# Optimization experiments

Measured on AMD Instinct MI355X. Metric: run time of the kernel, lower is better.

## Reference

```python
import jax, jax.numpy as jnp
import numpy as np
import math

B, L, D, H = 4, 1024, 512, 8
TAU = 0.1
LN_EPS = 1e-5


def _attn(xq, xk, xv, wq, bq, wk, bk, wv, bv, wo, bo, energy=None, threshold=None):
    Bq, Lq, Dm = xq.shape
    Dh = Dm // H
    Q = (xq @ wq.T + bq).reshape(Bq, Lq, H, Dh)
    K = (xk @ wk.T + bk).reshape(Bq, -1, H, Dh)
    V = (xv @ wv.T + bv).reshape(Bq, -1, H, Dh)
    sc = jnp.einsum('bqhd,bkhd->bhqk', Q, K) / jnp.sqrt(jnp.float32(Dh))
    if energy is not None:
        # mask keys whose mean |energy| over channels is below threshold
        mask = jnp.abs(energy).mean(-1)[:, None, None, :] > threshold  # (B,1,1,Lk)
        sc = jnp.where(mask, sc, -jnp.inf)
    w = jnp.nan_to_num(jax.nn.softmax(sc, axis=-1))  # nan->0 for fully-masked rows
    o = jnp.einsum('bhqk,bkhd->bqhd', w, V).reshape(Bq, Lq, Dm)
    return o @ wo.T + bo


def _ln(x, w, b):
    m = x.mean(-1, keepdims=True)
    v = x.var(-1, keepdims=True)
    return (x - m) / jnp.sqrt(v + LN_EPS) * w + b


def _mlp(x, w1, b1, w2, b2):
    h = jax.nn.gelu(x @ w1.T + b1, approximate=False)  # torch nn.GELU default = exact
    return h @ w2.T + b2


def setup_inputs():
    key = jax.random.key(0)
    ks = list(jax.random.split(key, 64))

    def nxt():
        return ks.pop(0)

    def w(shape, scale=0.02):
        return jax.random.normal(nxt(), shape, dtype=jnp.float32) * scale

    inp = {
        'LL': jax.random.normal(nxt(), (B, D, L), dtype=jnp.float32),
        'LH': jax.random.normal(nxt(), (B, D, L), dtype=jnp.float32),
        'raw_tau': jnp.float32(math.log(TAU / (1.0 - TAU))),
    }
    for p in ('llA', 'lhA', 'crA'):
        for nm in ('q', 'k', 'v', 'o'):
            inp[f'{p}_w{nm}'] = w((D, D))
            inp[f'{p}_b{nm}'] = jnp.zeros((D,), jnp.float32)
    for p in ('mlp_ll', 'mlp_lh'):
        inp[f'{p}_w1'] = w((4 * D, D))
        inp[f'{p}_b1'] = jnp.zeros((4 * D,), jnp.float32)
        inp[f'{p}_w2'] = w((D, 4 * D))
        inp[f'{p}_b2'] = jnp.zeros((D,), jnp.float32)
    inp['n1_w'] = jnp.ones((D,), jnp.float32)
    inp['n1_b'] = jnp.zeros((D,), jnp.float32)
    inp['n2_w'] = jnp.ones((D,), jnp.float32)
    inp['n2_b'] = jnp.zeros((D,), jnp.float32)
    return inp


def reference(LL, LH, raw_tau,
              llA_wq, llA_bq, llA_wk, llA_bk, llA_wv, llA_bv, llA_wo, llA_bo,
              lhA_wq, lhA_bq, lhA_wk, lhA_bk, lhA_wv, lhA_bv, lhA_wo, lhA_bo,
              crA_wq, crA_bq, crA_wk, crA_bk, crA_wv, crA_bv, crA_wo, crA_bo,
              mlp_ll_w1, mlp_ll_b1, mlp_ll_w2, mlp_ll_b2,
              mlp_lh_w1, mlp_lh_b1, mlp_lh_w2, mlp_lh_b2,
              n1_w, n1_b, n2_w, n2_b):
    tau = jax.nn.sigmoid(raw_tau)
    ll_s = jnp.transpose(LL, (0, 2, 1))  # (B,L,D)
    lh_s = jnp.transpose(LH, (0, 2, 1))
    ll_o = _attn(ll_s, ll_s, ll_s, llA_wq, llA_bq, llA_wk, llA_bk, llA_wv, llA_bv, llA_wo, llA_bo)
    lh_o = _attn(lh_s, lh_s, lh_s, lhA_wq, lhA_bq, lhA_wk, lhA_bk, lhA_wv, lhA_bv, lhA_wo, lhA_bo,
                 energy=lh_s, threshold=tau)
    cr_o = _attn(ll_o, lh_o, lh_o, crA_wq, crA_bq, crA_wk, crA_bk, crA_wv, crA_bv, crA_wo, crA_bo)
    ll_f = _ln(ll_s + ll_o + cr_o, n1_w, n1_b)
    ll_f = _mlp(ll_f, mlp_ll_w1, mlp_ll_b1, mlp_ll_w2, mlp_ll_b2) + ll_f
    lh_f = _ln(lh_s + lh_o, n2_w, n2_b)
    lh_f = _mlp(lh_f, mlp_lh_w1, mlp_lh_b1, mlp_lh_w2, mlp_lh_b2) + lh_f
    return (jnp.transpose(ll_f, (0, 2, 1)), jnp.transpose(lh_f, (0, 2, 1)))
```

## Files before the change

kernel.cpp:

```cpp
#include <hip/hip_runtime.h>
#include <hip/hip_bf16.h>
#include <stdint.h>

typedef unsigned short u16;
typedef __bf16 bf16_t;
typedef bf16_t bf16x8 __attribute__((ext_vector_type(8)));
typedef float f32x4 __attribute__((ext_vector_type(4)));

#define DEV static __device__ __forceinline__

DEV u16 f2b(float f) {
    __hip_bfloat16 h = __float2bfloat16(f);
    return __builtin_bit_cast(u16, h);
}

DEV bf16x8 ld_frag(const u16* p) {
    uint4 u = *reinterpret_cast<const uint4*>(p);
    return __builtin_bit_cast(bf16x8, u);
}

DEV float gelu(float v) {
    float y = 0.79788456080286536f * (v + 0.044715f * v * v * v);
    float e = __expf(-2.f * fabsf(y));
    float th = (1.f - e) / (1.f + e);
    th = copysignf(th, y);
    return 0.5f * v * (1.f + th);
}

DEV void gl_lds16(const u16* g, u16* l) {
    __builtin_amdgcn_global_load_lds(
        (const __attribute__((address_space(1))) void*)(uintptr_t)g,
        (__attribute__((address_space(3))) void*)(unsigned int)(uintptr_t)l,
        16, 0, 0);
}

struct ConvEnt { const float* s; u16* d; int n; };
struct CpyEnt { const float* s; float* d; };
struct PreArgs {
    const float* LL; const float* LH;
    float* llf; u16* llb; float* lhf; u16* lhb;
    ConvEnt ce[16];
    CpyEnt pe[8];
};

__global__ __launch_bounds__(256) void k_pre(PreArgs a) {
    __shared__ float tb[32][33];
    const int bid = blockIdx.x, t = threadIdx.x;
    if (bid < 4096) {
        const int z = bid >> 9, gy = (bid >> 5) & 15, gx = bid & 31;
        const int b = z & 3;
        const float* in = (z < 4) ? a.LL : a.LH;
        float* of = (z < 4) ? a.llf : a.lhf;
        u16* ob = (z < 4) ? a.llb : a.lhb;
        const int l0 = gx * 32, d0 = gy * 32;
        const int tx = t & 31, ty = t >> 5;
#pragma unroll
        for (int j = 0; j < 4; ++j) {
            int d = d0 + ty + j * 8;
            tb[ty + j * 8][tx] = in[((size_t)b * 512 + d) * 1024 + l0 + tx];
        }
        __syncthreads();
#pragma unroll
        for (int j = 0; j < 4; ++j) {
            int l = l0 + ty + j * 8;
            float v = tb[tx][ty + j * 8];
            size_t o = ((size_t)b * 1024 + l) * 512 + d0 + tx;
            of[o] = v;
            ob[o] = f2b(v);
        }
    } else if (bid < 8192) {
        const int cb = bid - 4096;
        const ConvEnt en = a.ce[cb >> 8];
        for (int i = ((cb & 255) * 256 + t) * 4; i < en.n; i += 256 * 256 * 4) {
            const float4 f = *reinterpret_cast<const float4*>(en.s + i);
            unsigned r0 = (unsigned)f2b(f.x) | ((unsigned)f2b(f.y) << 16);
            unsigned r1 = (unsigned)f2b(f.z) | ((unsigned)f2b(f.w) << 16);
            uint2 rr; rr.x = r0; rr.y = r1;
            *reinterpret_cast<uint2*>(en.d + i) = rr;
        }
    } else {
        const int cb = bid - 8192;
        const CpyEnt en = a.pe[cb >> 1];
        const int i = (cb & 1) * 256 + t;
        en.d[i] = en.s[i];
    }
}

__global__ __launch_bounds__(256) void k_tout(const float* __restrict__ y0, const float* __restrict__ y1,
                                              float* __restrict__ out) {
    __shared__ float tb[32][33];
    int z = blockIdx.z, b = z & 3;
    const float* in = (z < 4) ? y0 : y1;
    float* o = out + ((z < 4) ? 0 : (size_t)4096 * 512);
    int l0 = blockIdx.x * 32, d0 = blockIdx.y * 32;
    int tx = threadIdx.x, ty = threadIdx.y;
#pragma unroll
    for (int j = 0; j < 4; ++j) {
        int l = l0 + ty + j * 8;
        tb[ty + j * 8][tx] = in[((size_t)b * 1024 + l) * 512 + d0 + tx];
    }
    __syncthreads();
#pragma unroll
    for (int j = 0; j < 4; ++j) {
        int d = d0 + ty + j * 8;
        o[((size_t)b * 512 + d) * 1024 + l0 + tx] = tb[tx][ty + j * 8];
    }
}

__global__ __launch_bounds__(256) void k_mask(const float* __restrict__ lh_s,
                                              const float* __restrict__ raw_tau,
                                              float* __restrict__ kbias) {
    int row = blockIdx.x * 4 + (threadIdx.x >> 6);
    int lane = threadIdx.x & 63;
    const float* p = lh_s + (size_t)row * 512 + lane * 8;
    float s = 0.f;
#pragma unroll
    for (int j = 0; j < 8; ++j) s += fabsf(p[j]);
#pragma unroll
    for (int m = 32; m >= 1; m >>= 1) s += __shfl_xor(s, m, 64);
    float tau = 1.f / (1.f + expf(-raw_tau[0]));
    if (lane == 0) kbias[row] = (s * (1.f / 512.f) > tau) ? 0.f : -3.0e38f;
}

__global__ __launch_bounds__(256) void k_ln(const float* __restrict__ a, const float* __restrict__ b,
                                            const float* __restrict__ c, const float* __restrict__ w,
                                            const float* __restrict__ bi,
                                            float* __restrict__ of, u16* __restrict__ ob) {
    int row = blockIdx.x * 4 + (threadIdx.x >> 6);
    int lane = threadIdx.x & 63;
    size_t base = (size_t)row * 512 + lane * 8;
    float x[8];
#pragma unroll
    for (int j = 0; j < 8; ++j) {
        float v = a[base + j] + b[base + j];
        if (c) v += c[base + j];
        x[j] = v;
    }
    float s = 0.f, s2 = 0.f;
#pragma unroll
    for (int j = 0; j < 8; ++j) { s += x[j]; s2 += x[j] * x[j]; }
#pragma unroll
    for (int m = 32; m >= 1; m >>= 1) { s += __shfl_xor(s, m, 64); s2 += __shfl_xor(s2, m, 64); }
    float mean = s * (1.f / 512.f);
    float var = s2 * (1.f / 512.f) - mean * mean;
    float rs = rsqrtf(var + 1e-5f);
#pragma unroll
    for (int j = 0; j < 8; ++j) {
        float y = (x[j] - mean) * rs * w[lane * 8 + j] + bi[lane * 8 + j];
        of[base + j] = y;
        ob[base + j] = f2b(y);
    }
}

struct GP {
    const u16* A; const u16* W; const float* bias; const float* res;
    float* Cf; u16* Cb; u16* Qp; u16* Kp; u16* Vt;
    int N, K, kB, vB, nwg;
};

template <int BM, int BN, int GELU_ACT, int PACK>
__global__ __launch_bounds__(256) void k_gemm(GP p0, GP p1, int M) {
    constexpr int BK = 64;
    __shared__ alignas(16) u16 Al[2][BM * BK];
    __shared__ alignas(16) u16 Wl[2][BN * BK];
    GP g = (blockIdx.y == 0) ? p0 : p1;
    const int orig = blockIdx.x;
    if (orig >= g.nwg) return;
    int bid;
    {
        const int xcd = orig & 7, lin = orig >> 3;
        const int q = g.nwg >> 3, r = g.nwg & 7;
        bid = (xcd < r ? xcd * (q + 1) : r * (q + 1) + (xcd - r) * q) + lin;
    }
    const int K = g.K, N = g.N;
    const int nny = N / BN;
    const int m0 = (bid / nny) * BM, n0 = (bid % nny) * BN;

    const int t = threadIdx.x, w = t >> 6, l = t & 63;
    constexpr int FM = BM / 32, FN = BN / 32;
    const int wr = w >> 1, wc = w & 1;
    const int lq = l & 15, lg = l >> 4;
    f32x4 acc[FM][FN] = {};

    const int srow = l >> 3, schunk = l & 7;
    auto stage = [&](int kcol, int buf) {
#pragma unroll
        for (int i = 0; i < BM / 32; ++i) {
            const int row = i * 32 + w * 8 + srow;
            gl_lds16(g.A + (size_t)(m0 + row) * K + kcol + ((schunk ^ (row & 7)) * 8),
                     &Al[buf][(i * 32 + w * 8) * BK]);
        }
#pragma unroll
        for (int i = 0; i < BN / 32; ++i) {
            const int row = i * 32 + w * 8 + srow;
            gl_lds16(g.W + (size_t)(n0 + row) * K + kcol + ((schunk ^ (row & 7)) * 8),
                     &Wl[buf][(i * 32 + w * 8) * BK]);
        }
    };

    stage(0, 0);
    const int KT = K / BK;
    for (int kt = 0; kt < KT; ++kt) {
        const int cur = kt & 1;
        __syncthreads();
        if (kt + 1 < KT) stage((kt + 1) * BK, cur ^ 1);
#pragma unroll
        for (int s = 0; s < 2; ++s) {
            bf16x8 af[FM], bw[FN];
#pragma unroll
            for (int i = 0; i < FM; ++i) {
                const int row = wr * (BM / 2) + i * 16 + lq;
                af[i] = ld_frag(&Al[cur][row * BK + (((s * 4 + lg) ^ (row & 7)) * 8)]);
            }
#pragma unroll
            for (int j = 0; j < FN; ++j) {
                const int row = wc * (BN / 2) + j * 16 + lq;
                bw[j] = ld_frag(&Wl[cur][row * BK + (((s * 4 + lg) ^ (row & 7)) * 8)]);
            }
#pragma unroll
            for (int i = 0; i < FM; ++i)
#pragma unroll
                for (int j = 0; j < FN; ++j)
                    acc[i][j] = __builtin_amdgcn_mfma_f32_16x16x32_bf16(af[i], bw[j], acc[i][j], 0, 0, 0);
        }
    }

    if (PACK && n0 >= g.vB) {
        u16* T = (u16*)Al;
        constexpr int CH = BM / 8, CMASK = CH - 1, SH = (CH == 16) ? 4 : 3;
        __syncthreads();
#pragma unroll
        for (int i = 0; i < FM; ++i) {
#pragma unroll
            for (int j = 0; j < FN; ++j) {
                const int ni = wc * (BN / 2) + j * 16 + lq;
                const float bn = g.bias[n0 + ni];
#pragma unroll
                for (int r2 = 0; r2 < 4; ++r2) {
                    const int mi = wr * (BM / 2) + i * 16 + lg * 4 + r2;
                    T[ni * BM + (((mi >> 3) ^ (ni & CMASK)) * 8) + (mi & 7)] = f2b(acc[i][j][r2] + bn);
                }
            }
        }
        __syncthreads();
        const int bb = m0 >> 10, mloc = m0 & 1023;
        const int mc = t & CMASK, nib = t >> SH;
        constexpr int RPP = 256 / CH;
#pragma unroll
        for (int p2 = 0; p2 < BN / RPP; ++p2) {
            const int ni = nib + p2 * RPP;
            uint4 u = *reinterpret_cast<const uint4*>(&T[ni * BM + ((mc ^ (ni & CMASK)) * 8)]);
            const int d = n0 - g.vB + ni;
            *reinterpret_cast<uint4*>(
                &g.Vt[((size_t)(bb * 8 + (d >> 6)) * 64 + (d & 63)) * 1024 + mloc + mc * 8]) = u;
        }
        return;
    }

#pragma unroll
    for (int i = 0; i < FM; ++i) {
#pragma unroll
        for (int j = 0; j < FN; ++j) {
            const int n = n0 + wc * (BN / 2) + j * 16 + lq;
            const float bn = g.bias[n];
#pragma unroll
            for (int r2 = 0; r2 < 4; ++r2) {
                const int m = m0 + wr * (BM / 2) + i * 16 + lg * 4 + r2;
                float v = acc[i][j][r2] + bn;
                if (GELU_ACT) v = gelu(v);
                if (PACK) {
                    const int bb = m >> 10, ll_ = m & 1023;
                    if (n >= g.kB) {
                        const int d = n - g.kB;
                        g.Kp[((size_t)(bb * 8 + (d >> 6)) * 1024 + ll_) * 64 + (d & 63)] = f2b(v);
                    } else {
                        g.Qp[((size_t)(bb * 8 + (n >> 6)) * 1024 + ll_) * 64 + (n & 63)] = f2b(v * 0.125f);
                    }
                } else {
                    size_t o = (size_t)m * N + n;
                    if (g.res) v += g.res[o];
                    if (g.Cf) g.Cf[o] = v;
                    if (g.Cb) g.Cb[o] = f2b(v);
                }
            }
        }
    }
}

__global__ __launch_bounds__(256) void k_attn(const u16* __restrict__ Qp, const u16* __restrict__ Kp,
                                              const u16* __restrict__ Vtp, u16* __restrict__ O,
                                              const float* __restrict__ kbias, int nwg) {
    constexpr int L = 1024;
    __shared__ alignas(16) u16 Kl[2][64 * 64];
    __shared__ alignas(16) u16 Vl[2][64 * 64];
    __shared__ alignas(16) u16 Pl[128 * 64];
    const int t = threadIdx.x, w = t >> 6, l = t & 63;
    const int bid = ((int)blockIdx.x & 7) * (nwg >> 3) + ((int)blockIdx.x >> 3);
    const int bh = bid >> 3, q0 = (bid & 7) * 128;
    const int bz = bh >> 3, h = bh & 7;
    const int lq = l & 15, lg = l >> 4;
    const float* kb = (kbias != nullptr && bz >= 4) ? (kbias + (size_t)(bz - 4) * L) : nullptr;

    bf16x8 qa[2][2];
#pragma unroll
    for (int i = 0; i < 2; ++i) {
        const u16* qp = Qp + ((size_t)bh * L + q0 + w * 32 + i * 16 + lq) * 64 + lg * 8;
        qa[i][0] = ld_frag(qp);
        qa[i][1] = ld_frag(qp + 32);
    }

    const int r0 = w * 16 + (l >> 3), r1 = r0 + 8, c = l & 7;
    const u16* Ksrc0 = Kp + (size_t)bh * L * 64 + (size_t)r0 * 64 + ((c ^ (r0 & 7)) * 8);
    const u16* Ksrc1 = Kp + (size_t)bh * L * 64 + (size_t)r1 * 64 + ((c ^ (r1 & 7)) * 8);
    const u16* Vsrc0 = Vtp + (size_t)bh * 64 * L + (size_t)r0 * L + ((c ^ (r0 & 7)) * 8);
    const u16* Vsrc1 = Vtp + (size_t)bh * 64 * L + (size_t)r1 * L + ((c ^ (r1 & 7)) * 8);

    auto stage = [&](int k0, int buf) {
        gl_lds16(Ksrc0 + (size_t)k0 * 64, &Kl[buf][(w * 16) * 64]);
        gl_lds16(Ksrc1 + (size_t)k0 * 64, &Kl[buf][(w * 16 + 8) * 64]);
        gl_lds16(Vsrc0 + k0, &Vl[buf][(w * 16) * 64]);
        gl_lds16(Vsrc1 + k0, &Vl[buf][(w * 16 + 8) * 64]);
    };

    int addrA[4][2];
#pragma unroll
    for (int f = 0; f < 4; ++f) {
        int row = f * 16 + lq;
#pragma unroll
        for (int s = 0; s < 2; ++s) addrA[f][s] = row * 64 + (((s * 4 + lg) ^ (row & 7)) * 8);
    }
    int pwr[2][4], paddr[2][2];
#pragma unroll
    for (int i = 0; i < 2; ++i) {
        const int q = w * 32 + i * 16 + lq;
#pragma unroll
        for (int f = 0; f < 4; ++f) {
            const int chunk = f * 2 + (lg >> 1);
            pwr[i][f] = q * 64 + ((chunk ^ (lq & 7)) * 8) + (lg & 1) * 4;
        }
#pragma unroll
        for (int s = 0; s < 2; ++s) paddr[i][s] = q * 64 + (((s * 4 + lg) ^ (lq & 7)) * 8);
    }

    f32x4 oacc[2][4] = {};
    float lsum[2] = {0.f, 0.f};

    stage(0, 0);
    for (int kt = 0; kt < 16; ++kt) {
        const int cur = kt & 1;
        __syncthreads();
        if (kt + 1 < 16) stage((kt + 1) * 64, cur ^ 1);

        f32x4 sc[2][4];
#pragma unroll
        for (int f = 0; f < 4; ++f) {
            bf16x8 k0 = ld_frag(&Kl[cur][addrA[f][0]]);
            bf16x8 k1 = ld_frag(&Kl[cur][addrA[f][1]]);
#pragma unroll
            for (int i = 0; i < 2; ++i) {
                f32x4 a = {};
                a = __builtin_amdgcn_mfma_f32_16x16x32_bf16(k0, qa[i][0], a, 0, 0, 0);
                a = __builtin_amdgcn_mfma_f32_16x16x32_bf16(k1, qa[i][1], a, 0, 0, 0);
                sc[i][f] = a;
            }
        }
#pragma unroll
        for (int f = 0; f < 4; ++f) {
            float4 bv4;
            if (kb) bv4 = *reinterpret_cast<const float4*>(kb + kt * 64 + f * 16 + lg * 4);
            else { bv4.x = 0.f; bv4.y = 0.f; bv4.z = 0.f; bv4.w = 0.f; }
#pragma unroll
            for (int i = 0; i < 2; ++i) {
                float p0 = __expf(sc[i][f][0] + bv4.x);
                float p1 = __expf(sc[i][f][1] + bv4.y);
                float p2 = __expf(sc[i][f][2] + bv4.z);
                float p3 = __expf(sc[i][f][3] + bv4.w);
                lsum[i] += (p0 + p1) + (p2 + p3);
                uint2 pk;
                pk.x = (unsigned)f2b(p0) | ((unsigned)f2b(p1) << 16);
                pk.y = (unsigned)f2b(p2) | ((unsigned)f2b(p3) << 16);
                *reinterpret_cast<uint2*>(&Pl[pwr[i][f]]) = pk;
            }
        }
        bf16x8 pa[2][2];
#pragma unroll
        for (int i = 0; i < 2; ++i) {
            pa[i][0] = ld_frag(&Pl[paddr[i][0]]);
            pa[i][1] = ld_frag(&Pl[paddr[i][1]]);
        }
#pragma unroll
        for (int db = 0; db < 4; ++db) {
            bf16x8 v0 = ld_frag(&Vl[cur][addrA[db][0]]);
            bf16x8 v1 = ld_frag(&Vl[cur][addrA[db][1]]);
#pragma unroll
            for (int i = 0; i < 2; ++i) {
                oacc[i][db] = __builtin_amdgcn_mfma_f32_16x16x32_bf16(pa[i][0], v0, oacc[i][db], 0, 0, 0);
                oacc[i][db] = __builtin_amdgcn_mfma_f32_16x16x32_bf16(pa[i][1], v1, oacc[i][db], 0, 0, 0);
            }
        }
    }
#pragma unroll
    for (int i = 0; i < 2; ++i) {
        float v = lsum[i];
        v += __shfl_xor(v, 16, 64);
        v += __shfl_xor(v, 32, 64);
        lsum[i] = v;
    }
#pragma unroll
    for (int i = 0; i < 2; ++i) {
        float inv[4];
#pragma unroll
        for (int r = 0; r < 4; ++r) {
            float den = __shfl(lsum[i], lg * 4 + r, 64);
            inv[r] = (den > 0.f) ? 1.f / den : 0.f;
        }
#pragma unroll
        for (int db = 0; db < 4; ++db) {
#pragma unroll
            for (int r = 0; r < 4; ++r) {
                O[((size_t)bz * L + q0 + w * 32 + i * 16 + lg * 4 + r) * 512 + h * 64 + db * 16 + lq] =
                    f2b(oacc[i][db][r] * inv[r]);
            }
        }
    }
}

extern "C" void kernel_launch(void* const* d_in, const int* in_sizes, int n_in,
                              void* d_out, int out_size, void* d_ws, size_t ws_size,
                              hipStream_t stream) {
    const int M = 4096;
    const float* LL = (const float*)d_in[0];
    const float* LH = (const float*)d_in[1];
    const float* raw_tau = (const float*)d_in[2];
    auto F = [&](int i) { return (const float*)d_in[i]; };
    const int BIG = 1 << 28;

    char* p = (char*)d_ws;
    auto alloc = [&](size_t bytes) { void* r = (void*)p; p += (bytes + 255) & ~(size_t)255; return r; };
    const size_t MDf = (size_t)M * 512 * 4, MDb = (size_t)M * 512 * 2;
    float* ll_s_f = (float*)alloc(MDf);
    float* lh_s_f = (float*)alloc(MDf);
    u16* ll_s_b = (u16*)alloc(MDb);
    u16* lh_s_b = (u16*)alloc(MDb);
    u16* Qp = (u16*)alloc(2 * MDb);
    u16* Kp = (u16*)alloc(2 * MDb);
    u16* Vt = (u16*)alloc(2 * MDb);
    u16* Cxb = (u16*)alloc(2 * MDb);
    float* ll_o_f = (float*)alloc(MDf);
    u16* ll_o_b = (u16*)alloc(MDb);
    float* lh_o_f = (float*)alloc(MDf);
    u16* lh_o_b = (u16*)alloc(MDb);
    float* cr_o_f = (float*)alloc(MDf);
    float* ln_f_ll = (float*)alloc(MDf);
    float* ln_f_lh = (float*)alloc(MDf);
    u16* ln_b = (u16*)alloc(MDb);
    u16* hb = (u16*)alloc((size_t)M * 2048 * 2);
    float* yf_ll = (float*)alloc(MDf);
    float* yf_lh = (float*)alloc(MDf);
    float* kbias = (float*)alloc(4096 * 4);
    float* bqkv_ll = (float*)alloc(1536 * 4);
    float* bqkv_lh = (float*)alloc(1536 * 4);
    float* bkv_cr = (float*)alloc(1024 * 4);
    const size_t WDD = (size_t)262144;
    u16* wqkv_ll = (u16*)alloc(3 * WDD * 2);
    u16* wqkv_lh = (u16*)alloc(3 * WDD * 2);
    u16* wkv_cr = (u16*)alloc(2 * WDD * 2);
    u16* wq_cr = (u16*)alloc(WDD * 2);
    u16* wo_ll = (u16*)alloc(WDD * 2);
    u16* wo_lh = (u16*)alloc(WDD * 2);
    u16* wo_cr = (u16*)alloc(WDD * 2);
    u16* wm[4];
    for (int i = 0; i < 4; ++i) wm[i] = (u16*)alloc((size_t)1048576 * 2);

    const size_t SET = (size_t)4 * 8 * 1024 * 64;

    PreArgs pa;
    pa.LL = LL; pa.LH = LH;
    pa.llf = ll_s_f; pa.llb = ll_s_b; pa.lhf = lh_s_f; pa.lhb = lh_s_b;
    pa.ce[0] = {F(3), wqkv_ll, (int)WDD};
    pa.ce[1] = {F(5), wqkv_ll + WDD, (int)WDD};
    pa.ce[2] = {F(7), wqkv_ll + 2 * WDD, (int)WDD};
    pa.ce[3] = {F(11), wqkv_lh, (int)WDD};
    pa.ce[4] = {F(13), wqkv_lh + WDD, (int)WDD};
    pa.ce[5] = {F(15), wqkv_lh + 2 * WDD, (int)WDD};
    pa.ce[6] = {F(19), wq_cr, (int)WDD};
    pa.ce[7] = {F(21), wkv_cr, (int)WDD};
    pa.ce[8] = {F(23), wkv_cr + WDD, (int)WDD};
    pa.ce[9] = {F(9), wo_ll, (int)WDD};
    pa.ce[10] = {F(17), wo_lh, (int)WDD};
    pa.ce[11] = {F(25), wo_cr, (int)WDD};
    pa.ce[12] = {F(27), wm[0], 1048576};
    pa.ce[13] = {F(29), wm[1], 1048576};
    pa.ce[14] = {F(31), wm[2], 1048576};
    pa.ce[15] = {F(33), wm[3], 1048576};
    pa.pe[0] = {F(4), bqkv_ll};
    pa.pe[1] = {F(6), bqkv_ll + 512};
    pa.pe[2] = {F(8), bqkv_ll + 1024};
    pa.pe[3] = {F(12), bqkv_lh};
    pa.pe[4] = {F(14), bqkv_lh + 512};
    pa.pe[5] = {F(16), bqkv_lh + 1024};
    pa.pe[6] = {F(22), bkv_cr};
    pa.pe[7] = {F(24), bkv_cr + 512};
    k_pre<<<dim3(8208), 256, 0, stream>>>(pa);
    k_mask<<<dim3(1024), 256, 0, stream>>>(lh_s_f, raw_tau, kbias);

    auto gp = [&](const u16* A, const u16* W, const float* bias, int N, int K, int nwg) {
        GP g = {};
        g.A = A; g.W = W; g.bias = bias; g.N = N; g.K = K; g.nwg = nwg;
        g.kB = BIG; g.vB = BIG;
        return g;
    };

    {
        GP a = gp(ll_s_b, wqkv_ll, bqkv_ll, 1536, 512, 384);
        a.kB = 512; a.vB = 1024; a.Qp = Qp; a.Kp = Kp; a.Vt = Vt;
        GP b = gp(lh_s_b, wqkv_lh, bqkv_lh, 1536, 512, 384);
        b.kB = 512; b.vB = 1024; b.Qp = Qp + SET; b.Kp = Kp + SET; b.Vt = Vt + SET;
        k_gemm<128, 128, 0, 1><<<dim3(384, 2), 256, 0, stream>>>(a, b, M);
    }
    k_attn<<<dim3(512), 256, 0, stream>>>(Qp, Kp, Vt, Cxb, kbias, 512);
    {
        GP a = gp(Cxb, wo_ll, F(10), 512, 512, 512);
        a.Cf = ll_o_f; a.Cb = ll_o_b;
        GP b = gp(Cxb + SET, wo_lh, F(18), 512, 512, 512);
        b.Cf = lh_o_f; b.Cb = lh_o_b;
        k_gemm<64, 64, 0, 0><<<dim3(512, 2), 256, 0, stream>>>(a, b, M);
    }
    k_ln<<<dim3(1024), 256, 0, stream>>>(lh_s_f, lh_o_f, nullptr, F(37), F(38), ln_f_lh, ln_b);
    {
        GP a = gp(ln_b, wm[2], F(32), 2048, 512, 512);
        a.Cb = hb;
        k_gemm<128, 128, 1, 0><<<dim3(512, 1), 256, 0, stream>>>(a, a, M);
    }
    {
        GP a = gp(ll_o_b, wq_cr, F(20), 512, 512, 512);
        a.Qp = Qp;
        GP b = gp(lh_o_b, wkv_cr, bkv_cr, 1024, 512, 1024);
        b.kB = 0; b.vB = 512; b.Kp = Kp; b.Vt = Vt;
        k_gemm<64, 64, 0, 1><<<dim3(1024, 2), 256, 0, stream>>>(a, b, M);
    }
    k_attn<<<dim3(256), 256, 0, stream>>>(Qp, Kp, Vt, Cxb, nullptr, 256);
    {
        GP a = gp(Cxb, wo_cr, F(26), 512, 512, 512);
        a.Cf = cr_o_f;
        GP b = gp(hb, wm[3], F(34), 512, 2048, 512);
        b.Cf = yf_lh; b.res = ln_f_lh;
        k_gemm<64, 64, 0, 0><<<dim3(512, 2), 256, 0, stream>>>(a, b, M);
    }
    k_ln<<<dim3(1024), 256, 0, stream>>>(ll_s_f, ll_o_f, cr_o_f, F(35), F(36), ln_f_ll, ln_b);
    {
        GP a = gp(ln_b, wm[0], F(28), 2048, 512, 512);
        a.Cb = hb;
        k_gemm<128, 128, 1, 0><<<dim3(512, 1), 256, 0, stream>>>(a, a, M);
    }
    {
        GP a = gp(hb, wm[1], F(30), 512, 2048, 512);
        a.Cf = yf_ll; a.res = ln_f_ll;
        k_gemm<64, 64, 0, 0><<<dim3(512, 1), 256, 0, stream>>>(a, a, M);
    }
    k_tout<<<dim3(32, 16, 8), dim3(32, 8), 0, stream>>>(yf_ll, yf_lh, (float*)d_out);
}
```

Measured before the change: 261.7 us.

## Fuse mask into pre kernel, merge GEMM launches, write transposed output from GEMM

```diff
diff --git a/kernel.cpp b/kernel.cpp
--- a/kernel.cpp
+++ b/kernel.cpp
@@ -39,6 +39,7 @@
 struct PreArgs {
     const float* LL; const float* LH;
     float* llf; u16* llb; float* lhf; u16* lhb;
+    const float* raw_tau; float* kbias;
     ConvEnt ce[16];
     CpyEnt pe[8];
 };
@@ -78,48 +79,27 @@
             uint2 rr; rr.x = r0; rr.y = r1;
             *reinterpret_cast<uint2*>(en.d + i) = rr;
         }
-    } else {
+    } else if (bid < 8208) {
         const int cb = bid - 8192;
         const CpyEnt en = a.pe[cb >> 1];
         const int i = (cb & 1) * 256 + t;
         en.d[i] = en.s[i];
-    }
-}
-
-__global__ __launch_bounds__(256) void k_tout(const float* __restrict__ y0, const float* __restrict__ y1,
-                                              float* __restrict__ out) {
-    __shared__ float tb[32][33];
-    int z = blockIdx.z, b = z & 3;
-    const float* in = (z < 4) ? y0 : y1;
-    float* o = out + ((z < 4) ? 0 : (size_t)4096 * 512);
-    int l0 = blockIdx.x * 32, d0 = blockIdx.y * 32;
-    int tx = threadIdx.x, ty = threadIdx.y;
-#pragma unroll
-    for (int j = 0; j < 4; ++j) {
-        int l = l0 + ty + j * 8;
-        tb[ty + j * 8][tx] = in[((size_t)b * 1024 + l) * 512 + d0 + tx];
-    }
-    __syncthreads();
-#pragma unroll
-    for (int j = 0; j < 4; ++j) {
-        int d = d0 + ty + j * 8;
-        o[((size_t)b * 512 + d) * 1024 + l0 + tx] = tb[tx][ty + j * 8];
-    }
-}
-
-__global__ __launch_bounds__(256) void k_mask(const float* __restrict__ lh_s,
-                                              const float* __restrict__ raw_tau,
-                                              float* __restrict__ kbias) {
-    int row = blockIdx.x * 4 + (threadIdx.x >> 6);
-    int lane = threadIdx.x & 63;
-    const float* p = lh_s + (size_t)row * 512 + lane * 8;
-    float s = 0.f;
-#pragma unroll
-    for (int j = 0; j < 8; ++j) s += fabsf(p[j]);
-#pragma unroll
-    for (int m = 32; m >= 1; m >>= 1) s += __shfl_xor(s, m, 64);
-    float tau = 1.f / (1.f + expf(-raw_tau[0]));
-    if (lane == 0) kbias[row] = (s * (1.f / 512.f) > tau) ? 0.f : -3.0e38f;
+    } else {
+        const int cb = bid - 8208;
+        const int b = cb >> 4, k = (cb & 15) * 64 + (t & 63);
+        const int dg = t >> 6;
+        float s = 0.f;
+        for (int d = dg * 128; d < dg * 128 + 128; ++d)
+            s += fabsf(a.LH[((size_t)b * 512 + d) * 1024 + k]);
+        float* ps = &tb[0][0];
+        ps[dg * 64 + (t & 63)] = s;
+        __syncthreads();
+        if (t < 64) {
+            float tot = ps[t] + ps[64 + t] + ps[128 + t] + ps[192 + t];
+            float tau = 1.f / (1.f + expf(-a.raw_tau[0]));
+            a.kbias[b * 1024 + (cb & 15) * 64 + t] = (tot * (1.f / 512.f) > tau) ? 0.f : -3.0e38f;
+        }
+    }
 }
 
 __global__ __launch_bounds__(256) void k_ln(const float* __restrict__ a, const float* __restrict__ b,
@@ -154,16 +134,16 @@
 
 struct GP {
     const u16* A; const u16* W; const float* bias; const float* res;
-    float* Cf; u16* Cb; u16* Qp; u16* Kp; u16* Vt;
-    int N, K, kB, vB, nwg;
+    float* Cf; u16* Cb; float* Ct; u16* Qp; u16* Kp; u16* Vt;
+    int N, K, kB, vB, nwg, gelu, pack;
 };
 
-template <int BM, int BN, int GELU_ACT, int PACK>
-__global__ __launch_bounds__(256) void k_gemm(GP p0, GP p1, int M) {
+template <int BM, int BN>
+__global__ __launch_bounds__(256) void k_gemm(GP p0, GP p1, GP p2, int M) {
     constexpr int BK = 64;
     __shared__ alignas(16) u16 Al[2][BM * BK];
     __shared__ alignas(16) u16 Wl[2][BN * BK];
-    GP g = (blockIdx.y == 0) ? p0 : p1;
+    GP g = (blockIdx.y == 0) ? p0 : (blockIdx.y == 1) ? p1 : p2;
     const int orig = blockIdx.x;
     if (orig >= g.nwg) return;
     int bid;
@@ -225,7 +205,7 @@
         }
     }
 
-    if (PACK && n0 >= g.vB) {
+    if (g.pack && n0 >= g.vB) {
         u16* T = (u16*)Al;
         constexpr int CH = BM / 8, CMASK = CH - 1, SH = (CH == 16) ? 4 : 3;
         __syncthreads();
@@ -263,20 +243,39 @@
         for (int j = 0; j < FN; ++j) {
             const int n = n0 + wc * (BN / 2) + j * 16 + lq;
             const float bn = g.bias[n];
+            const int mb = m0 + wr * (BM / 2) + i * 16 + lg * 4;
+            float vv[4];
 #pragma unroll
             for (int r2 = 0; r2 < 4; ++r2) {
-                const int m = m0 + wr * (BM / 2) + i * 16 + lg * 4 + r2;
                 float v = acc[i][j][r2] + bn;
-                if (GELU_ACT) v = gelu(v);
-                if (PACK) {
+                if (g.gelu) v = gelu(v);
+                vv[r2] = v;
+            }
+            if (g.pack) {
+#pragma unroll
+                for (int r2 = 0; r2 < 4; ++r2) {
+                    const int m = mb + r2;
                     const int bb = m >> 10, ll_ = m & 1023;
                     if (n >= g.kB) {
                         const int d = n - g.kB;
-                        g.Kp[((size_t)(bb * 8 + (d >> 6)) * 1024 + ll_) * 64 + (d & 63)] = f2b(v);
+                        g.Kp[((size_t)(bb * 8 + (d >> 6)) * 1024 + ll_) * 64 + (d & 63)] = f2b(vv[r2]);
                     } else {
-                        g.Qp[((size_t)(bb * 8 + (n >> 6)) * 1024 + ll_) * 64 + (n & 63)] = f2b(v * 0.125f);
+                        g.Qp[((size_t)(bb * 8 + (n >> 6)) * 1024 + ll_) * 64 + (n & 63)] = f2b(vv[r2] * 0.125f);
                     }
-                } else {
+                }
+            } else if (g.Ct) {
+                float4 o4;
+                o4.x = vv[0] + (g.res ? g.res[(size_t)(mb + 0) * N + n] : 0.f);
+                o4.y = vv[1] + (g.res ? g.res[(size_t)(mb + 1) * N + n] : 0.f);
+                o4.z = vv[2] + (g.res ? g.res[(size_t)(mb + 2) * N + n] : 0.f);
+                o4.w = vv[3] + (g.res ? g.res[(size_t)(mb + 3) * N + n] : 0.f);
+                *reinterpret_cast<float4*>(
+                    &g.Ct[((size_t)(mb >> 10) * 512 + n) * 1024 + (mb & 1023)]) = o4;
+            } else {
+#pragma unroll
+                for (int r2 = 0; r2 < 4; ++r2) {
+                    const int m = mb + r2;
+                    float v = vv[r2];
                     size_t o = (size_t)m * N + n;
                     if (g.res) v += g.res[o];
                     if (g.Cf) g.Cf[o] = v;
@@ -455,8 +454,6 @@
     float* ln_f_lh = (float*)alloc(MDf);
     u16* ln_b = (u16*)alloc(MDb);
     u16* hb = (u16*)alloc((size_t)M * 2048 * 2);
-    float* yf_ll = (float*)alloc(MDf);
-    float* yf_lh = (float*)alloc(MDf);
     float* kbias = (float*)alloc(4096 * 4);
     float* bqkv_ll = (float*)alloc(1536 * 4);
     float* bqkv_lh = (float*)alloc(1536 * 4);
@@ -477,6 +474,7 @@
     PreArgs pa;
     pa.LL = LL; pa.LH = LH;
     pa.llf = ll_s_f; pa.llb = ll_s_b; pa.lhf = lh_s_f; pa.lhb = lh_s_b;
+    pa.raw_tau = raw_tau; pa.kbias = kbias;
     pa.ce[0] = {F(3), wqkv_ll, (int)WDD};
     pa.ce[1] = {F(5), wqkv_ll + WDD, (int)WDD};
     pa.ce[2] = {F(7), wqkv_ll + 2 * WDD, (int)WDD};
@@ -501,8 +499,7 @@
     pa.pe[5] = {F(16), bqkv_lh + 1024};
     pa.pe[6] = {F(22), bkv_cr};
     pa.pe[7] = {F(24), bkv_cr + 512};
-    k_pre<<<dim3(8208), 256, 0, stream>>>(pa);
-    k_mask<<<dim3(1024), 256, 0, stream>>>(lh_s_f, raw_tau, kbias);
+    k_pre<<<dim3(8272), 256, 0, stream>>>(pa);
 
     auto gp = [&](const u16* A, const u16* W, const float* bias, int N, int K, int nwg) {
         GP g = {};
@@ -513,10 +510,10 @@
 
     {
         GP a = gp(ll_s_b, wqkv_ll, bqkv_ll, 1536, 512, 384);
-        a.kB = 512; a.vB = 1024; a.Qp = Qp; a.Kp = Kp; a.Vt = Vt;
+        a.pack = 1; a.kB = 512; a.vB = 1024; a.Qp = Qp; a.Kp = Kp; a.Vt = Vt;
         GP b = gp(lh_s_b, wqkv_lh, bqkv_lh, 1536, 512, 384);
-        b.kB = 512; b.vB = 1024; b.Qp = Qp + SET; b.Kp = Kp + SET; b.Vt = Vt + SET;
-        k_gemm<128, 128, 0, 1><<<dim3(384, 2), 256, 0, stream>>>(a, b, M);
+        b.pack = 1; b.kB = 512; b.vB = 1024; b.Qp = Qp + SET; b.Kp = Kp + SET; b.Vt = Vt + SET;
+        k_gemm<128, 128><<<dim3(384, 2), 256, 0, stream>>>(a, b, b, M);
     }
     k_attn<<<dim3(512), 256, 0, stream>>>(Qp, Kp, Vt, Cxb, kbias, 512);
     {
@@ -524,39 +521,35 @@
         a.Cf = ll_o_f; a.Cb = ll_o_b;
         GP b = gp(Cxb + SET, wo_lh, F(18), 512, 512, 512);
         b.Cf = lh_o_f; b.Cb = lh_o_b;
-        k_gemm<64, 64, 0, 0><<<dim3(512, 2), 256, 0, stream>>>(a, b, M);
+        k_gemm<64, 64><<<dim3(512, 2), 256, 0, stream>>>(a, b, b, M);
     }
     k_ln<<<dim3(1024), 256, 0, stream>>>(lh_s_f, lh_o_f, nullptr, F(37), F(38), ln_f_lh, ln_b);
     {
-        GP a = gp(ln_b, wm[2], F(32), 2048, 512, 512);
-        a.Cb = hb;
-        k_gemm<128, 128, 1, 0><<<dim3(512, 1), 256, 0, stream>>>(a, a, M);
-    }
-    {
-        GP a = gp(ll_o_b, wq_cr, F(20), 512, 512, 512);
-        a.Qp = Qp;
-        GP b = gp(lh_o_b, wkv_cr, bkv_cr, 1024, 512, 1024);
-        b.kB = 0; b.vB = 512; b.Kp = Kp; b.Vt = Vt;
-        k_gemm<64, 64, 0, 1><<<dim3(1024, 2), 256, 0, stream>>>(a, b, M);
+        GP a = gp(ln_b, wm[2], F(32), 2048, 512, 1024);
+        a.gelu = 1; a.Cb = hb;
+        GP b = gp(ll_o_b, wq_cr, F(20), 512, 512, 256);
+        b.pack = 1; b.Qp = Qp;
+        GP cd = gp(lh_o_b, wkv_cr, bkv_cr, 1024, 512, 512);
+        cd.pack = 1; cd.kB = 0; cd.vB = 512; cd.Kp = Kp; cd.Vt = Vt;
+        k_gemm<128, 64><<<dim3(1024, 3), 256, 0, stream>>>(a, b, cd, M);
     }
     k_attn<<<dim3(256), 256, 0, stream>>>(Qp, Kp, Vt, Cxb, nullptr, 256);
     {
         GP a = gp(Cxb, wo_cr, F(26), 512, 512, 512);
         a.Cf = cr_o_f;
         GP b = gp(hb, wm[3], F(34), 512, 2048, 512);
-        b.Cf = yf_lh; b.res = ln_f_lh;
-        k_gemm<64, 64, 0, 0><<<dim3(512, 2), 256, 0, stream>>>(a, b, M);
+        b.res = ln_f_lh; b.Ct = (float*)d_out + (size_t)4096 * 512;
+        k_gemm<64, 64><<<dim3(512, 2), 256, 0, stream>>>(a, b, b, M);
     }
     k_ln<<<dim3(1024), 256, 0, stream>>>(ll_s_f, ll_o_f, cr_o_f, F(35), F(36), ln_f_ll, ln_b);
     {
         GP a = gp(ln_b, wm[0], F(28), 2048, 512, 512);
-        a.Cb = hb;
-        k_gemm<128, 128, 1, 0><<<dim3(512, 1), 256, 0, stream>>>(a, a, M);
+        a.gelu = 1; a.Cb = hb;
+        k_gemm<128, 128><<<dim3(512, 1), 256, 0, stream>>>(a, a, a, M);
     }
     {
         GP a = gp(hb, wm[1], F(30), 512, 2048, 512);
-        a.Cf = yf_ll; a.res = ln_f_ll;
-        k_gemm<64, 64, 0, 0><<<dim3(512, 1), 256, 0, stream>>>(a, a, M);
-    }
-    k_tout<<<dim3(32, 16, 8), dim3(32, 8), 0, stream>>>(yf_ll, yf_lh, (float*)d_out);
-}
+        a.res = ln_f_ll; a.Ct = (float*)d_out;
+        k_gemm<64, 64><<<dim3(512, 1), 256, 0, stream>>>(a, a, a, M);
+    }
+}
```

Result: slower. 283.8 us (+8.4%).
